# Kernel optimization log

Measured on AMD Instinct MI355X. Metric: run time of the kernel, lower is better.

The kernel has to match this reference:

```python
import jax, jax.numpy as jnp
import numpy as np

D_MODEL = 1024
NUM_MODULES = 8
MAX_TRANSLATION = 3.0
MAX_ROT_ANGLE = 3.141592653589793


def setup_inputs() -> dict:
    key = jax.random.key(0)
    k1, k2, k3, k4 = jax.random.split(key, 4)
    B, N = 8, 8192
    node_feats = jax.random.normal(k1, (B, N, D_MODEL), jnp.float32)
    coords = jax.random.normal(k2, (B, N, 3), jnp.float32)
    W = jax.random.normal(k3, (NUM_MODULES * 8, D_MODEL), jnp.float32) * (1.0 / np.sqrt(D_MODEL))
    b = jax.random.normal(k4, (NUM_MODULES * 8,), jnp.float32) * 0.01
    return {"node_feats": node_feats, "coords": coords, "W": W, "b": b}


def _normalize(x, eps=1e-12):
    return x / jnp.clip(jnp.linalg.norm(x, axis=-1, keepdims=True), eps)


def _axis_angle_to_quaternion(aa):
    # pytorch3d convention: quat = [cos(theta/2), axis * sin(theta/2)]
    angles = jnp.linalg.norm(aa, axis=-1, keepdims=True)
    half = angles * 0.5
    small = jnp.abs(angles) < 1e-6
    safe_angles = jnp.where(small, 1.0, angles)
    sin_half_over_angle = jnp.where(small, 0.5 - angles * angles / 48.0, jnp.sin(half) / safe_angles)
    return jnp.concatenate([jnp.cos(half), aa * sin_half_over_angle], axis=-1)


def _quat_mul(a, b):
    aw, ax, ay, az = a[..., 0], a[..., 1], a[..., 2], a[..., 3]
    bw, bx, by, bz = b[..., 0], b[..., 1], b[..., 2], b[..., 3]
    ow = aw * bw - ax * bx - ay * by - az * bz
    ox = aw * bx + ax * bw + ay * bz - az * by
    oy = aw * by - ax * bz + ay * bw + az * bx
    oz = aw * bz + ax * by - ay * bx + az * bw
    return jnp.stack([ow, ox, oy, oz], axis=-1)


def _quat_apply(q, p):
    # q: [B,1,4], p: [B,N,3] -> rotate points: im(q * (0,p) * q^-1)
    pq = jnp.concatenate([jnp.zeros_like(p[..., :1]), p], axis=-1)
    q_inv = q * jnp.array([1.0, -1.0, -1.0, -1.0], q.dtype)
    return _quat_mul(_quat_mul(q, pq), q_inv)[..., 1:]


def reference(node_feats, coords, W, b):
    B, N, _ = coords.shape
    params = (node_feats @ W.T + b).reshape(B, N, NUM_MODULES, 8)
    anchor_logits = params[..., 0:1]   # [B,N,M,1]
    select_logits = params[..., 1:2]
    rot_axis = params[..., 2:5]
    trans = params[..., 5:8]

    anchor_w = jax.nn.softmax(anchor_logits, axis=1)      # softmax over N
    select_p = jax.nn.sigmoid(select_logits)

    angles = jnp.linalg.norm(rot_axis, axis=-1, keepdims=True)
    axis_n = _normalize(rot_axis)
    angles = jnp.tanh(angles) * MAX_ROT_ANGLE
    quats = _axis_angle_to_quaternion(axis_n * angles)    # [B,N,M,4]
    trans = jnp.tanh(trans) * MAX_TRANSLATION             # [B,N,M,3]

    xs = (jnp.moveaxis(quats, 2, 0),     # [M,B,N,4]
          jnp.moveaxis(trans, 2, 0),     # [M,B,N,3]
          jnp.moveaxis(anchor_w, 2, 0),  # [M,B,N,1]
          jnp.moveaxis(select_p, 2, 0))  # [M,B,N,1]

    def step(c, per):
        q, t, aw, sp = per
        anchor = jnp.sum(c * aw, axis=1, keepdims=True)               # [B,1,3]
        s = jnp.clip(jnp.sum(sp, axis=1, keepdims=True), 1e-8)        # [B,1,1]
        q_group = _normalize(jnp.sum(q * sp, axis=1, keepdims=True) / s)  # [B,1,4]
        t_group = jnp.sum(t * sp, axis=1, keepdims=True) / s          # [B,1,3]
        moved = _quat_apply(q_group, c - anchor) + anchor + t_group   # [B,N,3]
        return c + sp * (moved - c), None                             # lerp

    out, _ = jax.lax.scan(step, coords, xs)
    return out
```

## Files before the change

kernel.cpp:

```cpp
#include <hip/hip_runtime.h>
#include <hip/hip_bf16.h>
#include <hip/hip_fp16.h>
#include <math.h>

#define D_MODEL 1024
#define NMOD 8
#define BATCH 8
#define NNODE 8192
#define PI_F 3.14159265358979323846f
#define MAXT 3.0f

typedef short bf16x8 __attribute__((ext_vector_type(8)));
typedef float f32x4 __attribute__((ext_vector_type(4)));

__device__ inline unsigned short f2bf(float x) {
    __hip_bfloat16 h = __float2bfloat16(x);
    return __builtin_bit_cast(unsigned short, h);
}
__device__ inline float h2f(unsigned short u) {
    __half h = __builtin_bit_cast(__half, u);
    return __half2float(h);
}
__device__ inline unsigned short f2h(float x) {
    __half h = __float2half(x);
    return __builtin_bit_cast(unsigned short, h);
}

__global__ void pack_b(const float* __restrict__ W, unsigned short* __restrict__ Bpk,
                       int* __restrict__ cnt) {
    int t = blockIdx.x * 256 + threadIdx.x;
    if (t < BATCH) cnt[t] = 0;
    int l  = t & 63;
    int g  = (t >> 6) & 3;
    int ks = t >> 8;
    int j  = g * 16 + (l & 15);
    int k0 = ks * 32 + ((l >> 4) * 8);
    const float* wp = &W[(size_t)j * D_MODEL + k0];
    bf16x8 pack;
    #pragma unroll
    for (int r = 0; r < 8; ++r) pack[r] = (short)f2bf(wp[r]);
    *reinterpret_cast<bf16x8*>(Bpk + (size_t)t * 8) = pack;
}

__device__ __forceinline__ void loadg2(float4 (&dst)[4], const float* arow, int g) {
    #pragma unroll
    for (int i = 0; i < 2; ++i) {
        dst[2 * i]     = *reinterpret_cast<const float4*>(arow + (g * 2 + i) * 32);
        dst[2 * i + 1] = *reinterpret_cast<const float4*>(arow + (g * 2 + i) * 32 + 4);
    }
}

__global__ __launch_bounds__(1024) void fused(
    const float* __restrict__ feats, const unsigned short* __restrict__ Bpk,
    const float* __restrict__ bias, const float* __restrict__ coords,
    unsigned int* __restrict__ esp,
    float* __restrict__ partials,
    int* __restrict__ cnt,
    float* __restrict__ out)
{
    __shared__ __align__(16) unsigned char smem[131072];
    const int bid  = blockIdx.x;
    const int tid  = threadIdx.x;
    const int lane = tid & 63;
    const int wv   = tid >> 6;

    if (bid < 256) {
        {
            const char* gsrc = (const char*)Bpk;
            #pragma unroll
            for (int r = 0; r < 8; ++r) {
                const int off = r * 16384 + wv * 1024;
                __builtin_amdgcn_global_load_lds(
                    (const __attribute__((address_space(1))) unsigned int*)(gsrc + off + lane * 16),
                    (__attribute__((address_space(3))) unsigned int*)(smem + off),
                    16, 0, 0);
            }
        }

        const int mt    = bid * 16 + wv;
        const int mbase = mt * 16;
        const float* arow = feats + (size_t)(mbase + (lane & 15)) * D_MODEL + ((lane >> 4) * 8);
        const unsigned short* Blds = (const unsigned short*)smem;

        f32x4 acc[4];
        #pragma unroll
        for (int g = 0; g < 4; ++g) acc[g] = (f32x4){0.f, 0.f, 0.f, 0.f};

        float4 Ab[4][4];
        #pragma unroll
        for (int i = 0; i < 4; ++i) loadg2(Ab[i], arow, i);

        __syncthreads();

        #pragma unroll
        for (int i = 0; i < 16; ++i) {
            {
                const float4 (&src)[4] = Ab[i & 3];
                #pragma unroll
                for (int ii = 0; ii < 2; ++ii) {
                    float f[8] = {src[2*ii].x, src[2*ii].y, src[2*ii].z, src[2*ii].w,
                                  src[2*ii+1].x, src[2*ii+1].y, src[2*ii+1].z, src[2*ii+1].w};
                    bf16x8 a;
                    #pragma unroll
                    for (int j = 0; j < 8; ++j) a[j] = (short)f2bf(f[j]);
                    const int ks = i * 2 + ii;
                    #pragma unroll
                    for (int gg = 0; gg < 4; ++gg) {
                        bf16x8 bh = *reinterpret_cast<const bf16x8*>(
                            Blds + ((size_t)((ks * 4 + gg) * 64 + lane)) * 8);
                        acc[gg] = __builtin_amdgcn_mfma_f32_16x16x32_bf16(a, bh, acc[gg], 0, 0, 0);
                    }
                }
            }
            if (i + 4 < 16) loadg2(Ab[i & 3], arow, i + 4);
        }

        __syncthreads();
        float* pbuf = reinterpret_cast<float*>(smem) + (size_t)wv * (16 * 68);
        float* sacc = reinterpret_cast<float*>(smem + 69632);
        if (tid < 64) sacc[tid] = 0.f;

        #pragma unroll
        for (int g = 0; g < 4; ++g) {
            float bj = bias[g * 16 + (lane & 15)];
            #pragma unroll
            for (int r = 0; r < 4; ++r)
                pbuf[((lane >> 4) * 4 + r) * 68 + g * 16 + (lane & 15)] = acc[g][r] + bj;
        }
        __syncthreads();

        const int b    = mbase >> 13;
        const int nInB = mbase & 8191;

        #pragma unroll
        for (int h = 0; h < 2; ++h) {
            const int node = lane & 15;
            const int m    = (lane >> 4) + 4 * h;
            const float* pa = &pbuf[node * 68 + m * 8];
            float al = pa[0], sl = pa[1];
            float ax = pa[2], ay = pa[3], az = pa[4];
            float tx = pa[5], ty = pa[6], tz = pa[7];

            float ew = expf(al);
            float sp = 1.f / (1.f + expf(-sl));

            float n0  = sqrtf(ax * ax + ay * ay + az * az);
            float inv = 1.f / fmaxf(n0, 1e-12f);
            float ang = tanhf(n0) * PI_F;
            float hf  = 0.5f * ang;
            float shoa = (ang < 1e-6f) ? (0.5f - ang * ang * (1.f / 48.f))
                                       : (sinf(hf) / ang);
            float qw = cosf(hf);
            float fac = inv * ang * shoa;
            float qx = ax * fac, qy = ay * fac, qz = az * fac;

            float ttx = tanhf(tx) * MAXT, tty = tanhf(ty) * MAXT, ttz = tanhf(tz) * MAXT;

            size_t base = ((size_t)(b * NMOD + m)) * NNODE + nInB + node;
            esp[base] = ((unsigned)f2h(sp) << 16) | (unsigned)f2h(ew);

            float red[8];
            red[0] = sp;
            red[1] = sp * qw; red[2] = sp * qx; red[3] = sp * qy; red[4] = sp * qz;
            red[5] = sp * ttx; red[6] = sp * tty; red[7] = sp * ttz;
            #pragma unroll
            for (int v = 0; v < 8; ++v) {
                #pragma unroll
                for (int o = 1; o < 16; o <<= 1) red[v] += __shfl_xor(red[v], o);
            }
            if ((lane & 15) == 0) {
                #pragma unroll
                for (int v = 0; v < 8; ++v) atomicAdd(&sacc[m * 8 + v], red[v]);
            }
        }
        __syncthreads();

        if (tid < 64) {
            partials[((size_t)b * 32 + (bid & 31)) * 64 + tid] = sacc[tid];
            __threadfence();
            if (tid == 0)
                __hip_atomic_fetch_add(&cnt[b], 1, __ATOMIC_RELEASE, __HIP_MEMORY_SCOPE_AGENT);
        }
    } else {
        const int b = bid - 256;
        float* redbuf = reinterpret_cast<float*>(smem);
        float* bcast  = reinterpret_cast<float*>(smem) + 64;
        float* smod   = reinterpret_cast<float*>(smem) + 96;

        const int n0 = tid * 8;
        const int wid = wv;

        float cx[8], cy[8], cz[8];
        {
            float c[24];
            const float4* cp4 = reinterpret_cast<const float4*>(
                &coords[((size_t)b * NNODE + n0) * 3]);
            #pragma unroll
            for (int q = 0; q < 6; ++q) {
                float4 v = cp4[q];
                c[q * 4 + 0] = v.x; c[q * 4 + 1] = v.y;
                c[q * 4 + 2] = v.z; c[q * 4 + 3] = v.w;
            }
            #pragma unroll
            for (int i = 0; i < 8; ++i) { cx[i] = c[3*i]; cy[i] = c[3*i+1]; cz[i] = c[3*i+2]; }
        }

        if (tid == 0) {
            while (__hip_atomic_load(&cnt[b], __ATOMIC_ACQUIRE, __HIP_MEMORY_SCOPE_AGENT) < 32)
                __builtin_amdgcn_s_sleep(8);
        }
        __syncthreads();

        if (tid < 64) {
            float s = 0.f;
            #pragma unroll 4
            for (int blk = 0; blk < 32; ++blk)
                s += partials[((size_t)b * 32 + blk) * 64 + tid];
            smod[tid] = s;
        }
        __syncthreads();

        const uint4* esp4 = reinterpret_cast<const uint4*>(&esp[(size_t)b * NMOD * NNODE]);
        uint4 cur0 = esp4[(0 * NNODE + n0) >> 2];
        uint4 cur1 = esp4[((0 * NNODE + n0) >> 2) + 1];

        for (int m = 0; m < NMOD; ++m) {
            const int mn = (m + 1 < NMOD) ? m + 1 : m;
            uint4 nxt0 = esp4[(mn * NNODE + n0) >> 2];
            uint4 nxt1 = esp4[((mn * NNODE + n0) >> 2) + 1];

            unsigned pk[8] = {cur0.x, cur0.y, cur0.z, cur0.w, cur1.x, cur1.y, cur1.z, cur1.w};
            float ev[8], spl[8];
            #pragma unroll
            for (int i = 0; i < 8; ++i) {
                ev[i]  = h2f((unsigned short)(pk[i] & 0xFFFFu));
                spl[i] = h2f((unsigned short)(pk[i] >> 16));
            }

            float se = 0.f, sx = 0.f, sy = 0.f, sz = 0.f;
            #pragma unroll
            for (int i = 0; i < 8; ++i) {
                se += ev[i]; sx += ev[i] * cx[i]; sy += ev[i] * cy[i]; sz += ev[i] * cz[i];
            }
            float vals[4] = {se, sx, sy, sz};
            #pragma unroll
            for (int v = 0; v < 4; ++v) {
                float x = vals[v];
                #pragma unroll
                for (int o = 32; o > 0; o >>= 1) x += __shfl_down(x, o);
                if (lane == 0) redbuf[wid * 4 + v] = x;
            }
            __syncthreads();
            if (wid == 0) {
                float x = redbuf[lane];
                x += __shfl_down(x, 32);
                x += __shfl_down(x, 16);
                x += __shfl_down(x, 8);
                x += __shfl_down(x, 4);
                if (lane < 4) bcast[lane] = x;
            }
            __syncthreads();
            const float SE = bcast[0];
            const float AXc = bcast[1] / SE, AYc = bcast[2] / SE, AZc = bcast[3] / SE;

            const float* sm = &smod[m * 8];
            float s  = fmaxf(sm[0], 1e-8f);
            float qw = sm[1] / s, qx = sm[2] / s, qy = sm[3] / s, qz = sm[4] / s;
            float qn = sqrtf(qw * qw + qx * qx + qy * qy + qz * qz);
            float qi = 1.f / fmaxf(qn, 1e-12f);
            qw *= qi; qx *= qi; qy *= qi; qz *= qi;

            float xx = qx*qx, yy = qy*qy, zz = qz*qz;
            float xy = qx*qy, xz = qx*qz, yz = qy*qz;
            float wx = qw*qx, wy = qw*qy, wz = qw*qz;
            float r00 = 1.f - 2.f*(yy+zz), r01 = 2.f*(xy-wz),       r02 = 2.f*(xz+wy);
            float r10 = 2.f*(xy+wz),       r11 = 1.f - 2.f*(xx+zz), r12 = 2.f*(yz-wx);
            float r20 = 2.f*(xz-wy),       r21 = 2.f*(yz+wx),       r22 = 1.f - 2.f*(xx+yy);
            float dx = AXc + sm[5] / s, dy = AYc + sm[6] / s, dz = AZc + sm[7] / s;

            #pragma unroll
            for (int i = 0; i < 8; ++i) {
                float px = cx[i] - AXc, py = cy[i] - AYc, pz = cz[i] - AZc;
                float mx = fmaf(r00, px, fmaf(r01, py, fmaf(r02, pz, dx)));
                float my = fmaf(r10, px, fmaf(r11, py, fmaf(r12, pz, dy)));
                float mz = fmaf(r20, px, fmaf(r21, py, fmaf(r22, pz, dz)));
                float sp = spl[i];
                cx[i] = fmaf(sp, mx - cx[i], cx[i]);
                cy[i] = fmaf(sp, my - cy[i], cy[i]);
                cz[i] = fmaf(sp, mz - cz[i], cz[i]);
            }
            cur0 = nxt0; cur1 = nxt1;
            __syncthreads();
        }

        {
            float c[24];
            #pragma unroll
            for (int i = 0; i < 8; ++i) { c[3*i] = cx[i]; c[3*i+1] = cy[i]; c[3*i+2] = cz[i]; }
            float4* op4 = reinterpret_cast<float4*>(&out[((size_t)b * NNODE + n0) * 3]);
            #pragma unroll
            for (int q = 0; q < 6; ++q)
                op4[q] = make_float4(c[q*4+0], c[q*4+1], c[q*4+2], c[q*4+3]);
        }
    }
}

extern "C" void kernel_launch(void* const* d_in, const int* in_sizes, int n_in,
                              void* d_out, int out_size, void* d_ws, size_t ws_size,
                              hipStream_t stream) {
    const float* feats  = (const float*)d_in[0];
    const float* coords = (const float*)d_in[1];
    const float* W      = (const float*)d_in[2];
    const float* bias   = (const float*)d_in[3];
    float* out = (float*)d_out;

    char* ws = (char*)d_ws;
    unsigned short* Bpk = (unsigned short*)(ws);
    unsigned int* esp   = (unsigned int*)(ws + 262144);
    float* partials     = (float*)(ws + 262144 + 2097152);
    int* cnt            = (int*)(ws + 262144 + 2097152 + 65536);

    pack_b<<<32, 256, 0, stream>>>(W, Bpk, cnt);
    fused<<<264, 1024, 0, stream>>>(feats, Bpk, bias, coords, esp, partials, cnt, out);
}
```

Before: 96.02 us.

## Fold weight packing into fused kernel and run scan in first GEMM block

Removes the separate pack_b launch: every block now reads the fp32 W, converts it to bf16 in the MFMA fragment layout and writes it to LDS itself. The 8 dedicated scan blocks are gone; the first GEMM block of each batch runs the sequential module scan after its own tile. The reset-counter handshake becomes per-block token flags. The aim is to cut a launch and the idle scan blocks. The cost is redundant W conversion in all 256 blocks. The flags are never cleared, so on repeated calls stale tokens could let the scan read partials before they are rewritten.

```diff
diff --git a/kernel.cpp b/kernel.cpp
--- a/kernel.cpp
+++ b/kernel.cpp
@@ -9,6 +9,7 @@
 #define NNODE 8192
 #define PI_F 3.14159265358979323846f
 #define MAXT 3.0f
+#define TOKEN 0x1CEB00DAu
 
 typedef short bf16x8 __attribute__((ext_vector_type(8)));
 typedef float f32x4 __attribute__((ext_vector_type(4)));
@@ -26,22 +27,6 @@
     return __builtin_bit_cast(unsigned short, h);
 }
 
-__global__ void pack_b(const float* __restrict__ W, unsigned short* __restrict__ Bpk,
-                       int* __restrict__ cnt) {
-    int t = blockIdx.x * 256 + threadIdx.x;
-    if (t < BATCH) cnt[t] = 0;
-    int l  = t & 63;
-    int g  = (t >> 6) & 3;
-    int ks = t >> 8;
-    int j  = g * 16 + (l & 15);
-    int k0 = ks * 32 + ((l >> 4) * 8);
-    const float* wp = &W[(size_t)j * D_MODEL + k0];
-    bf16x8 pack;
-    #pragma unroll
-    for (int r = 0; r < 8; ++r) pack[r] = (short)f2bf(wp[r]);
-    *reinterpret_cast<bf16x8*>(Bpk + (size_t)t * 8) = pack;
-}
-
 __device__ __forceinline__ void loadg2(float4 (&dst)[4], const float* arow, int g) {
     #pragma unroll
     for (int i = 0; i < 2; ++i) {
@@ -50,12 +35,32 @@
     }
 }
 
-__global__ __launch_bounds__(1024) void fused(
-    const float* __restrict__ feats, const unsigned short* __restrict__ Bpk,
+__device__ __forceinline__ void compg2(const float4 (&src)[4], int g,
+                                       const unsigned short* __restrict__ Blds, int lane,
+                                       f32x4 (&acc)[4]) {
+    #pragma unroll
+    for (int i = 0; i < 2; ++i) {
+        float f[8] = {src[2*i].x, src[2*i].y, src[2*i].z, src[2*i].w,
+                      src[2*i+1].x, src[2*i+1].y, src[2*i+1].z, src[2*i+1].w};
+        bf16x8 a;
+        #pragma unroll
+        for (int j = 0; j < 8; ++j) a[j] = (short)f2bf(f[j]);
+        const int ks = g * 2 + i;
+        #pragma unroll
+        for (int gg = 0; gg < 4; ++gg) {
+            bf16x8 bh = *reinterpret_cast<const bf16x8*>(
+                Blds + ((size_t)((ks * 4 + gg) * 64 + lane)) * 8);
+            acc[gg] = __builtin_amdgcn_mfma_f32_16x16x32_bf16(a, bh, acc[gg], 0, 0, 0);
+        }
+    }
+}
+
+__global__ __launch_bounds__(1024, 4) void fused(
+    const float* __restrict__ feats, const float* __restrict__ W,
     const float* __restrict__ bias, const float* __restrict__ coords,
     unsigned int* __restrict__ esp,
     float* __restrict__ partials,
-    int* __restrict__ cnt,
+    unsigned int* __restrict__ flags,
     float* __restrict__ out)
 {
     __shared__ __align__(16) unsigned char smem[131072];
@@ -64,129 +69,117 @@
     const int lane = tid & 63;
     const int wv   = tid >> 6;
 
-    if (bid < 256) {
-        {
-            const char* gsrc = (const char*)Bpk;
-            #pragma unroll
-            for (int r = 0; r < 8; ++r) {
-                const int off = r * 16384 + wv * 1024;
-                __builtin_amdgcn_global_load_lds(
-                    (const __attribute__((address_space(1))) unsigned int*)(gsrc + off + lane * 16),
-                    (__attribute__((address_space(3))) unsigned int*)(smem + off),
-                    16, 0, 0);
-            }
-        }
-
-        const int mt    = bid * 16 + wv;
-        const int mbase = mt * 16;
-        const float* arow = feats + (size_t)(mbase + (lane & 15)) * D_MODEL + ((lane >> 4) * 8);
-        const unsigned short* Blds = (const unsigned short*)smem;
-
-        f32x4 acc[4];
-        #pragma unroll
-        for (int g = 0; g < 4; ++g) acc[g] = (f32x4){0.f, 0.f, 0.f, 0.f};
-
-        float4 Ab[4][4];
-        #pragma unroll
-        for (int i = 0; i < 4; ++i) loadg2(Ab[i], arow, i);
-
-        __syncthreads();
-
-        #pragma unroll
-        for (int i = 0; i < 16; ++i) {
-            {
-                const float4 (&src)[4] = Ab[i & 3];
-                #pragma unroll
-                for (int ii = 0; ii < 2; ++ii) {
-                    float f[8] = {src[2*ii].x, src[2*ii].y, src[2*ii].z, src[2*ii].w,
-                                  src[2*ii+1].x, src[2*ii+1].y, src[2*ii+1].z, src[2*ii+1].w};
-                    bf16x8 a;
-                    #pragma unroll
-                    for (int j = 0; j < 8; ++j) a[j] = (short)f2bf(f[j]);
-                    const int ks = i * 2 + ii;
-                    #pragma unroll
-                    for (int gg = 0; gg < 4; ++gg) {
-                        bf16x8 bh = *reinterpret_cast<const bf16x8*>(
-                            Blds + ((size_t)((ks * 4 + gg) * 64 + lane)) * 8);
-                        acc[gg] = __builtin_amdgcn_mfma_f32_16x16x32_bf16(a, bh, acc[gg], 0, 0, 0);
-                    }
-                }
-            }
-            if (i + 4 < 16) loadg2(Ab[i & 3], arow, i + 4);
-        }
-
-        __syncthreads();
-        float* pbuf = reinterpret_cast<float*>(smem) + (size_t)wv * (16 * 68);
-        float* sacc = reinterpret_cast<float*>(smem + 69632);
-        if (tid < 64) sacc[tid] = 0.f;
-
-        #pragma unroll
-        for (int g = 0; g < 4; ++g) {
-            float bj = bias[g * 16 + (lane & 15)];
-            #pragma unroll
-            for (int r = 0; r < 4; ++r)
-                pbuf[((lane >> 4) * 4 + r) * 68 + g * 16 + (lane & 15)] = acc[g][r] + bj;
-        }
-        __syncthreads();
-
-        const int b    = mbase >> 13;
-        const int nInB = mbase & 8191;
-
-        #pragma unroll
-        for (int h = 0; h < 2; ++h) {
-            const int node = lane & 15;
-            const int m    = (lane >> 4) + 4 * h;
-            const float* pa = &pbuf[node * 68 + m * 8];
-            float al = pa[0], sl = pa[1];
-            float ax = pa[2], ay = pa[3], az = pa[4];
-            float tx = pa[5], ty = pa[6], tz = pa[7];
-
-            float ew = expf(al);
-            float sp = 1.f / (1.f + expf(-sl));
-
-            float n0  = sqrtf(ax * ax + ay * ay + az * az);
-            float inv = 1.f / fmaxf(n0, 1e-12f);
-            float ang = tanhf(n0) * PI_F;
-            float hf  = 0.5f * ang;
-            float shoa = (ang < 1e-6f) ? (0.5f - ang * ang * (1.f / 48.f))
-                                       : (sinf(hf) / ang);
-            float qw = cosf(hf);
-            float fac = inv * ang * shoa;
-            float qx = ax * fac, qy = ay * fac, qz = az * fac;
-
-            float ttx = tanhf(tx) * MAXT, tty = tanhf(ty) * MAXT, ttz = tanhf(tz) * MAXT;
-
-            size_t base = ((size_t)(b * NMOD + m)) * NNODE + nInB + node;
-            esp[base] = ((unsigned)f2h(sp) << 16) | (unsigned)f2h(ew);
-
-            float red[8];
-            red[0] = sp;
-            red[1] = sp * qw; red[2] = sp * qx; red[3] = sp * qy; red[4] = sp * qz;
-            red[5] = sp * ttx; red[6] = sp * tty; red[7] = sp * ttz;
-            #pragma unroll
-            for (int v = 0; v < 8; ++v) {
-                #pragma unroll
-                for (int o = 1; o < 16; o <<= 1) red[v] += __shfl_xor(red[v], o);
-            }
-            if ((lane & 15) == 0) {
-                #pragma unroll
-                for (int v = 0; v < 8; ++v) atomicAdd(&sacc[m * 8 + v], red[v]);
-            }
-        }
-        __syncthreads();
-
-        if (tid < 64) {
-            partials[((size_t)b * 32 + (bid & 31)) * 64 + tid] = sacc[tid];
-            __threadfence();
-            if (tid == 0)
-                __hip_atomic_fetch_add(&cnt[b], 1, __ATOMIC_RELEASE, __HIP_MEMORY_SCOPE_AGENT);
-        }
-    } else {
-        const int b = bid - 256;
-        float* redbuf = reinterpret_cast<float*>(smem);
-        float* bcast  = reinterpret_cast<float*>(smem) + 64;
-        float* smod   = reinterpret_cast<float*>(smem) + 96;
-
+    const int mt    = bid * 16 + wv;
+    const int mbase = mt * 16;
+    const float* arow = feats + (size_t)(mbase + (lane & 15)) * D_MODEL + ((lane >> 4) * 8);
+
+    f32x4 acc[4];
+    #pragma unroll
+    for (int g = 0; g < 4; ++g) acc[g] = (f32x4){0.f, 0.f, 0.f, 0.f};
+
+    float4 Ab[4][4];
+    #pragma unroll
+    for (int i = 0; i < 4; ++i) loadg2(Ab[i], arow, i);
+
+    {
+        unsigned short* Bl = (unsigned short*)smem;
+        #pragma unroll
+        for (int r = 0; r < 8; ++r) {
+            const int e  = r * 1024 + tid;
+            const int l  = e & 63;
+            const int g  = (e >> 6) & 3;
+            const int ks = e >> 8;
+            const int j  = g * 16 + (l & 15);
+            const int k0 = ks * 32 + ((l >> 4) * 8);
+            const float* wp = &W[(size_t)j * D_MODEL + k0];
+            const float4 w0 = *reinterpret_cast<const float4*>(wp);
+            const float4 w1 = *reinterpret_cast<const float4*>(wp + 4);
+            float f[8] = {w0.x, w0.y, w0.z, w0.w, w1.x, w1.y, w1.z, w1.w};
+            bf16x8 pk;
+            #pragma unroll
+            for (int q = 0; q < 8; ++q) pk[q] = (short)f2bf(f[q]);
+            *reinterpret_cast<bf16x8*>(Bl + (size_t)e * 8) = pk;
+        }
+    }
+    __syncthreads();
+
+    const unsigned short* Blds = (const unsigned short*)smem;
+    #pragma unroll
+    for (int i = 0; i < 16; ++i) {
+        compg2(Ab[i & 3], i, Blds, lane, acc);
+        if (i + 4 < 16) loadg2(Ab[i & 3], arow, i + 4);
+    }
+
+    __syncthreads();
+    float* pbuf = reinterpret_cast<float*>(smem) + (size_t)wv * (16 * 68);
+    float* sacc = reinterpret_cast<float*>(smem + 69632);
+    if (tid < 64) sacc[tid] = 0.f;
+
+    #pragma unroll
+    for (int g = 0; g < 4; ++g) {
+        float bj = bias[g * 16 + (lane & 15)];
+        #pragma unroll
+        for (int r = 0; r < 4; ++r)
+            pbuf[((lane >> 4) * 4 + r) * 68 + g * 16 + (lane & 15)] = acc[g][r] + bj;
+    }
+    __syncthreads();
+
+    const int b    = mbase >> 13;
+    const int nInB = mbase & 8191;
+
+    #pragma unroll
+    for (int h = 0; h < 2; ++h) {
+        const int node = lane & 15;
+        const int m    = (lane >> 4) + 4 * h;
+        const float* pa = &pbuf[node * 68 + m * 8];
+        float al = pa[0], sl = pa[1];
+        float ax = pa[2], ay = pa[3], az = pa[4];
+        float tx = pa[5], ty = pa[6], tz = pa[7];
+
+        float ew = expf(al);
+        float sp = 1.f / (1.f + expf(-sl));
+
+        float n0  = sqrtf(ax * ax + ay * ay + az * az);
+        float inv = 1.f / fmaxf(n0, 1e-12f);
+        float ang = tanhf(n0) * PI_F;
+        float hf  = 0.5f * ang;
+        float shoa = (ang < 1e-6f) ? (0.5f - ang * ang * (1.f / 48.f))
+                                   : (sinf(hf) / ang);
+        float qw = cosf(hf);
+        float fac = inv * ang * shoa;
+        float qx = ax * fac, qy = ay * fac, qz = az * fac;
+
+        float ttx = tanhf(tx) * MAXT, tty = tanhf(ty) * MAXT, ttz = tanhf(tz) * MAXT;
+
+        size_t base = ((size_t)(b * NMOD + m)) * NNODE + nInB + node;
+        esp[base] = ((unsigned)f2h(sp) << 16) | (unsigned)f2h(ew);
+
+        float red[8];
+        red[0] = sp;
+        red[1] = sp * qw; red[2] = sp * qx; red[3] = sp * qy; red[4] = sp * qz;
+        red[5] = sp * ttx; red[6] = sp * tty; red[7] = sp * ttz;
+        #pragma unroll
+        for (int v = 0; v < 8; ++v) {
+            #pragma unroll
+            for (int o = 1; o < 16; o <<= 1) red[v] += __shfl_xor(red[v], o);
+        }
+        if ((lane & 15) == 0) {
+            #pragma unroll
+            for (int v = 0; v < 8; ++v) atomicAdd(&sacc[m * 8 + v], red[v]);
+        }
+    }
+    __syncthreads();
+
+    if (tid < 64)
+        partials[((size_t)b * 32 + (bid & 31)) * 64 + tid] = sacc[tid];
+    __threadfence();
+    if (tid == 0)
+        __hip_atomic_store(&flags[b * 32 + (bid & 31)], TOKEN,
+                           __ATOMIC_RELEASE, __HIP_MEMORY_SCOPE_AGENT);
+
+    if ((bid & 31) != 0) return;
+
+    {
         const int n0 = tid * 8;
         const int wid = wv;
 
@@ -205,11 +198,16 @@
             for (int i = 0; i < 8; ++i) { cx[i] = c[3*i]; cy[i] = c[3*i+1]; cz[i] = c[3*i+2]; }
         }
 
-        if (tid == 0) {
-            while (__hip_atomic_load(&cnt[b], __ATOMIC_ACQUIRE, __HIP_MEMORY_SCOPE_AGENT) < 32)
+        if (tid < 32) {
+            while (__hip_atomic_load(&flags[b * 32 + tid],
+                                     __ATOMIC_ACQUIRE, __HIP_MEMORY_SCOPE_AGENT) != TOKEN)
                 __builtin_amdgcn_s_sleep(8);
         }
         __syncthreads();
+
+        float* smod   = reinterpret_cast<float*>(smem);
+        float* redbuf = reinterpret_cast<float*>(smem + 1024);
+        float* bcast  = reinterpret_cast<float*>(smem + 2048);
 
         if (tid < 64) {
             float s = 0.f;
@@ -315,11 +313,9 @@
     float* out = (float*)d_out;
 
     char* ws = (char*)d_ws;
-    unsigned short* Bpk = (unsigned short*)(ws);
-    unsigned int* esp   = (unsigned int*)(ws + 262144);
-    float* partials     = (float*)(ws + 262144 + 2097152);
-    int* cnt            = (int*)(ws + 262144 + 2097152 + 65536);
-
-    pack_b<<<32, 256, 0, stream>>>(W, Bpk, cnt);
-    fused<<<264, 1024, 0, stream>>>(feats, Bpk, bias, coords, esp, partials, cnt, out);
-}
+    unsigned int* esp   = (unsigned int*)(ws);
+    float* partials     = (float*)(ws + 2097152);
+    unsigned int* flags = (unsigned int*)(ws + 2097152 + 65536);
+
+    fused<<<256, 1024, 0, stream>>>(feats, W, bias, coords, esp, partials, flags, out);
+}
```

Measured after the change: 156.4 us. 62.8% more time.
